# Performance work log

Measured on AMD Instinct MI355X. Metric: run time of the kernel, lower is better.

The kernel has to match this reference:

```python
import jax, jax.numpy as jnp
import numpy as np

MARGIN = 0.2
SCALE = 30.0

def setup_inputs() -> dict:
    key = jax.random.key(0)
    k1, k2 = jax.random.split(key)
    B, D, C = 8192, 512, 100
    embeddings = jax.random.normal(k1, (B, D), dtype=jnp.float32)
    labels = jax.random.randint(k2, (B,), 0, C, dtype=jnp.int64)
    return {"embeddings": embeddings, "labels": labels}

def reference(embeddings, labels):
    # Cosine similarity via one GEMM: normalize rows once, then n @ n.T.
    # (torch F.cosine_similarity uses eps=1e-8 on norms)
    norms = jnp.maximum(jnp.linalg.norm(embeddings, axis=1, keepdims=True), 1e-8)
    n = embeddings / norms                      # [B, D]
    sim = n @ n.T                               # [B, B]
    pos_mask = labels[:, None] == labels[None, :]  # includes diagonal, as in original
    e = jnp.exp(SCALE * (sim - MARGIN))         # [B, B]
    pos_sum = jnp.sum(jnp.where(pos_mask, e, 0.0))
    neg_sum = jnp.sum(jnp.where(pos_mask, 0.0, e))
    loss = jnp.log1p(neg_sum / pos_sum)
    return loss
```

## Files before the change

kernel.cpp:

```cpp
#include <hip/hip_runtime.h>
#include <hip/hip_bf16.h>
#include <math.h>


#define BDIM 8192
#define DDIM 512
#define MARGIN 0.2f
#define SCALE 30.0f

#define BT 256
#define BK 32
#define NKT (DDIM / BK)
#define NT (BDIM / BT)
#define NBLK (NT * (NT + 1) / 2)

typedef __hip_bfloat16 bf16;
using f32x4  = __attribute__((ext_vector_type(4))) float;
using bf16x8 = __attribute__((ext_vector_type(8))) short;
using us8    = __attribute__((ext_vector_type(8))) unsigned short;

#define GLOAD_LDS16(gp, lp)                                                    \
    __builtin_amdgcn_global_load_lds(                                          \
        (const __attribute__((address_space(1))) unsigned int*)(gp),           \
        (__attribute__((address_space(3))) unsigned int*)(lp), 16, 0, 0)

__device__ __forceinline__ unsigned short f2bf(float x) {
    union { bf16 h; unsigned short u; } c;
    c.h = __float2bfloat16(x);
    return c.u;
}

__global__ __launch_bounds__(256)
void norm_rows_kernel(const float* __restrict__ emb, bf16* __restrict__ nout,
                      double* __restrict__ accum, unsigned* __restrict__ ctr) {
    if (blockIdx.x == 0 && threadIdx.x == 0) {
        accum[0] = 0.0; accum[1] = 0.0; *ctr = 0u;
    }
    const int row  = blockIdx.x * 4 + (threadIdx.x >> 6);
    const int lane = threadIdx.x & 63;
    const float4* src = (const float4*)(emb + (size_t)row * DDIM) + lane * 2;
    const float4 a = src[0];
    const float4 b = src[1];
    float ss = a.x * a.x + a.y * a.y + a.z * a.z + a.w * a.w
             + b.x * b.x + b.y * b.y + b.z * b.z + b.w * b.w;
    #pragma unroll
    for (int off = 1; off < 64; off <<= 1) ss += __shfl_xor(ss, off, 64);
    const float inv = 1.0f / fmaxf(sqrtf(ss), 1e-8f);
    float v[8] = { a.x, a.y, a.z, a.w, b.x, b.y, b.z, b.w };
    us8 o;
    #pragma unroll
    for (int i = 0; i < 8; ++i) o[i] = f2bf(v[i] * inv);
    *((us8*)(nout + (size_t)row * DDIM) + lane) = o;
}

__global__ __launch_bounds__(512, 2)
void gemm_loss_kernel(const bf16* __restrict__ nmat,
                      const int* __restrict__ labels,
                      double* __restrict__ accum, unsigned* __restrict__ ctr,
                      float* __restrict__ out) {
    const int hw = blockIdx.x;
    const int l = (hw & 7) * (NBLK / 8) + (hw >> 3);
    auto tri = [](int b) { return ((65 - b) * b) >> 1; };
    int bi = (int)((65.0 - sqrt(4225.0 - 8.0 * (double)l)) * 0.5);
    bi = bi < 0 ? 0 : (bi > 31 ? 31 : bi);
    while (bi > 0 && tri(bi) > l) --bi;
    while (tri(bi + 1) <= l) ++bi;
    const int bj = bi + (l - tri(bi));

    __shared__ alignas(16) short As[4][BT * BK];
    __shared__ alignas(16) short Bs[4][BT * BK];
    __shared__ int lr[BT], lc[BT];
    __shared__ double red[16];

    const int tix = threadIdx.x, wid = tix >> 6, lane = tix & 63;
    if (tix < 256) lr[tix] = labels[bi * BT + tix];
    else           lc[tix - 256] = labels[bj * BT + (tix - 256)];

    const int wm = wid >> 2;
    const int wn = wid & 3;

    const int srow = wid * 16 + (lane >> 2);
    const int scol = ((lane & 3) ^ ((lane >> 3) & 3)) * 8;
    const bf16* gA = nmat + (size_t)(bi * BT + srow) * DDIM + scol;
    const bf16* gB = nmat + (size_t)(bj * BT + srow) * DDIM + scol;
    const int ldst = wid * 16 * BK;

    #define STG_A(buf, kt, h)                                                  \
        GLOAD_LDS16(gA + (size_t)((h) * 128) * DDIM + (kt) * BK,               \
                    &As[buf][(h) * 128 * BK + ldst])
    #define STG_B(buf, kt, h)                                                  \
        GLOAD_LDS16(gB + (size_t)((h) * 128) * DDIM + (kt) * BK,               \
                    &Bs[buf][(h) * 128 * BK + ldst])

    const int aoff  = (lane & 15) * BK + (((lane >> 4) ^ ((lane >> 1) & 3)) * 8);
    const int abase = wm * 128 * BK;
    const int bbase = wn * 64 * BK;

    f32x4 acc[8][4] = {};

    #pragma unroll
    for (int tt = 0; tt < 3; ++tt) {
        STG_A(tt, tt, 0); STG_A(tt, tt, 1);
        STG_B(tt, tt, 0); STG_B(tt, tt, 1);
    }
    asm volatile("s_waitcnt vmcnt(8)" ::: "memory");
    __builtin_amdgcn_s_barrier();
    asm volatile("" ::: "memory");

    #pragma unroll
    for (int t = 0; t < NKT; ++t) {
        const int cur = t & 3, pre = (t + 3) & 3;
        bf16x8 a[4], b[4];
        #pragma unroll
        for (int m = 0; m < 4; ++m)
            a[m] = *(const bf16x8*)&As[cur][abase + m * (16 * BK) + aoff];
        #pragma unroll
        for (int n = 0; n < 4; ++n)
            b[n] = *(const bf16x8*)&Bs[cur][bbase + n * (16 * BK) + aoff];
        if (t < NKT - 3) { STG_A(pre, t + 3, 0); STG_A(pre, t + 3, 1); }
        __builtin_amdgcn_s_barrier();
        asm volatile("s_waitcnt lgkmcnt(0)" ::: "memory");
        __builtin_amdgcn_sched_barrier(0);
        __builtin_amdgcn_s_setprio(1);
        #pragma unroll
        for (int m = 0; m < 4; ++m)
            #pragma unroll
            for (int n = 0; n < 4; ++n)
                acc[m][n] = __builtin_amdgcn_mfma_f32_16x16x32_bf16(
                    a[m], b[n], acc[m][n], 0, 0, 0);
        __builtin_amdgcn_s_setprio(0);
        #pragma unroll
        for (int m = 0; m < 4; ++m)
            a[m] = *(const bf16x8*)&As[cur][abase + (m + 4) * (16 * BK) + aoff];
        if (t < NKT - 3) { STG_B(pre, t + 3, 0); STG_B(pre, t + 3, 1); }
        if (t <= NKT - 4)      { asm volatile("s_waitcnt vmcnt(8)" ::: "memory"); }
        else if (t == NKT - 3) { asm volatile("s_waitcnt vmcnt(4)" ::: "memory"); }
        else if (t == NKT - 2) { asm volatile("s_waitcnt vmcnt(0)" ::: "memory"); }
        __builtin_amdgcn_s_barrier();
        asm volatile("s_waitcnt lgkmcnt(0)" ::: "memory");
        __builtin_amdgcn_sched_barrier(0);
        __builtin_amdgcn_s_setprio(1);
        #pragma unroll
        for (int m = 0; m < 4; ++m)
            #pragma unroll
            for (int n = 0; n < 4; ++n)
                acc[m + 4][n] = __builtin_amdgcn_mfma_f32_16x16x32_bf16(
                    a[m], b[n], acc[m + 4][n], 0, 0, 0);
        __builtin_amdgcn_s_setprio(0);
    }
    #undef STG_A
    #undef STG_B

    float posf = 0.0f, negf = 0.0f;
    const int rbase = wm * 128 + (lane >> 4) * 4;
    const int cbase = wn * 64 + (lane & 15);
    #pragma unroll
    for (int m = 0; m < 8; ++m) {
        #pragma unroll
        for (int n = 0; n < 4; ++n) {
            const int ljv = lc[cbase + n * 16];
            #pragma unroll
            for (int r = 0; r < 4; ++r) {
                const float e = __expf(fmaf(acc[m][n][r], SCALE, -SCALE * MARGIN));
                if (lr[rbase + m * 16 + r] == ljv) posf += e; else negf += e;
            }
        }
    }

    double dp = (double)posf, dn = (double)negf;
    #pragma unroll
    for (int o = 32; o > 0; o >>= 1) {
        dp += __shfl_down(dp, o, 64);
        dn += __shfl_down(dn, o, 64);
    }
    if (lane == 0) { red[wid * 2] = dp; red[wid * 2 + 1] = dn; }
    __syncthreads();
    if (tix == 0) {
        const double w = (bi == bj) ? 1.0 : 2.0;
        double p = 0.0, q = 0.0;
        #pragma unroll
        for (int i = 0; i < 8; ++i) { p += red[2 * i]; q += red[2 * i + 1]; }
        atomicAdd(&accum[0], p * w);
        atomicAdd(&accum[1], q * w);
        __threadfence();
        unsigned prev = atomicAdd(ctr, 1u);
        if (prev == NBLK - 1) {
            __threadfence();
            double pp = atomicAdd(&accum[0], 0.0);
            double qq = atomicAdd(&accum[1], 0.0);
            out[0] = (float)log1p(qq / pp);
        }
    }
}

extern "C" void kernel_launch(void* const* d_in, const int* in_sizes, int n_in,
                              void* d_out, int out_size, void* d_ws, size_t ws_size,
                              hipStream_t stream) {
    const float* emb  = (const float*)d_in[0];
    const int* labels = (const int*)d_in[1];
    float* out        = (float*)d_out;

    double* accum = (double*)d_ws;
    unsigned* ctr = (unsigned*)((char*)d_ws + 16);
    bf16* nmat    = (bf16*)((char*)d_ws + 256);

    norm_rows_kernel<<<BDIM / 4, 256, 0, stream>>>(emb, nmat, accum, ctr);
    gemm_loss_kernel<<<NBLK, 512, 0, stream>>>(nmat, labels, accum, ctr, out);
}
```

Measured before the change: 134.7 us.

## Shrink GEMM tiles to 128x128 with single-buffered LDS and supertile block ordering

Changes the fused GEMM+loss kernel from 256x256 tiles with 512 threads and a 4-stage async LDS pipeline to 128x128 tiles with 256 threads and a simple load-sync-compute loop. Block indices are remapped in 16x16 supertile groups of the upper triangle, aiming for better L2 locality and more blocks for load balance. This gives up the prefetch pipeline and halves per-block data reuse, so global/LDS traffic per FLOP roughly doubles and load latency is exposed at every barrier.

Result: slower. 172.7 us (+28.2%).

```diff
diff --git a/kernel.cpp b/kernel.cpp
--- a/kernel.cpp
+++ b/kernel.cpp
@@ -8,10 +8,10 @@
 #define MARGIN 0.2f
 #define SCALE 30.0f
 
-#define BT 256
+#define BM 128
 #define BK 32
 #define NKT (DDIM / BK)
-#define NT (BDIM / BT)
+#define NT (BDIM / BM)
 #define NBLK (NT * (NT + 1) / 2)
 
 typedef __hip_bfloat16 bf16;
@@ -53,109 +53,83 @@
     *((us8*)(nout + (size_t)row * DDIM) + lane) = o;
 }
 
-__global__ __launch_bounds__(512, 2)
+__global__ __launch_bounds__(256)
 void gemm_loss_kernel(const bf16* __restrict__ nmat,
                       const int* __restrict__ labels,
                       double* __restrict__ accum, unsigned* __restrict__ ctr,
                       float* __restrict__ out) {
-    const int hw = blockIdx.x;
-    const int l = (hw & 7) * (NBLK / 8) + (hw >> 3);
-    auto tri = [](int b) { return ((65 - b) * b) >> 1; };
-    int bi = (int)((65.0 - sqrt(4225.0 - 8.0 * (double)l)) * 0.5);
-    bi = bi < 0 ? 0 : (bi > 31 ? 31 : bi);
-    while (bi > 0 && tri(bi) > l) --bi;
-    while (tri(bi + 1) <= l) ++bi;
-    const int bj = bi + (l - tri(bi));
+    const int p = (blockIdx.x & 7) * (NBLK / 8) + (blockIdx.x >> 3);
+    const int scum[10] = {136, 392, 648, 904, 1040, 1296, 1552, 1688, 1944, 2080};
+    const int ssi[10]  = {0, 0, 0, 0, 1, 1, 1, 2, 2, 3};
+    const int ssj[10]  = {0, 1, 2, 3, 1, 2, 3, 2, 3, 3};
+    int s = 0;
+    while (p >= scum[s]) ++s;
+    const int q = p - (s ? scum[s - 1] : 0);
+    int bi, bj;
+    if (ssi[s] == ssj[s]) {
+        int r = 0;
+        while ((16 * (r + 1) - ((r + 1) * r) / 2) <= q) ++r;
+        const int rowbase = 16 * r - (r * (r - 1)) / 2;
+        bi = ssi[s] * 16 + r;
+        bj = ssj[s] * 16 + r + (q - rowbase);
+    } else {
+        bi = ssi[s] * 16 + (q >> 4);
+        bj = ssj[s] * 16 + (q & 15);
+    }
 
-    __shared__ alignas(16) short As[4][BT * BK];
-    __shared__ alignas(16) short Bs[4][BT * BK];
-    __shared__ int lr[BT], lc[BT];
-    __shared__ double red[16];
+    __shared__ alignas(16) short As[BM * BK];
+    __shared__ alignas(16) short Bs[BM * BK];
+    __shared__ int lr[BM], lc[BM];
+    __shared__ double red[8];
 
-    const int tix = threadIdx.x, wid = tix >> 6, lane = tix & 63;
-    if (tix < 256) lr[tix] = labels[bi * BT + tix];
-    else           lc[tix - 256] = labels[bj * BT + (tix - 256)];
+    const int t = threadIdx.x, wid = t >> 6, lane = t & 63;
+    if (t < 128) lr[t] = labels[bi * BM + t];
+    else         lc[t - 128] = labels[bj * BM + (t - 128)];
 
-    const int wm = wid >> 2;
-    const int wn = wid & 3;
+    const int wr = wid >> 1;
+    const int wc = wid & 1;
 
-    const int srow = wid * 16 + (lane >> 2);
+    const int srow = 16 * wid + (lane >> 2);
     const int scol = ((lane & 3) ^ ((lane >> 3) & 3)) * 8;
-    const bf16* gA = nmat + (size_t)(bi * BT + srow) * DDIM + scol;
-    const bf16* gB = nmat + (size_t)(bj * BT + srow) * DDIM + scol;
-    const int ldst = wid * 16 * BK;
-
-    #define STG_A(buf, kt, h)                                                  \
-        GLOAD_LDS16(gA + (size_t)((h) * 128) * DDIM + (kt) * BK,               \
-                    &As[buf][(h) * 128 * BK + ldst])
-    #define STG_B(buf, kt, h)                                                  \
-        GLOAD_LDS16(gB + (size_t)((h) * 128) * DDIM + (kt) * BK,               \
-                    &Bs[buf][(h) * 128 * BK + ldst])
+    const bf16* gA = nmat + (size_t)(bi * BM + srow) * DDIM + scol;
+    const bf16* gB = nmat + (size_t)(bj * BM + srow) * DDIM + scol;
+    const int ldst = (16 * wid) * BK;
 
     const int aoff  = (lane & 15) * BK + (((lane >> 4) ^ ((lane >> 1) & 3)) * 8);
-    const int abase = wm * 128 * BK;
-    const int bbase = wn * 64 * BK;
+    const int abase = (wr * 64) * BK;
+    const int bbase = (wc * 64) * BK;
 
-    f32x4 acc[8][4] = {};
+    f32x4 acc[4][4] = {};
 
-    #pragma unroll
-    for (int tt = 0; tt < 3; ++tt) {
-        STG_A(tt, tt, 0); STG_A(tt, tt, 1);
-        STG_B(tt, tt, 0); STG_B(tt, tt, 1);
-    }
-    asm volatile("s_waitcnt vmcnt(8)" ::: "memory");
-    __builtin_amdgcn_s_barrier();
-    asm volatile("" ::: "memory");
+    for (int kt = 0; kt < NKT; ++kt) {
+        const int k0 = kt * BK;
+        GLOAD_LDS16(gA + k0,                    &As[ldst]);
+        GLOAD_LDS16(gA + (size_t)64 * DDIM + k0, &As[64 * BK + ldst]);
+        GLOAD_LDS16(gB + k0,                    &Bs[ldst]);
+        GLOAD_LDS16(gB + (size_t)64 * DDIM + k0, &Bs[64 * BK + ldst]);
+        __syncthreads();
 
-    #pragma unroll
-    for (int t = 0; t < NKT; ++t) {
-        const int cur = t & 3, pre = (t + 3) & 3;
         bf16x8 a[4], b[4];
         #pragma unroll
         for (int m = 0; m < 4; ++m)
-            a[m] = *(const bf16x8*)&As[cur][abase + m * (16 * BK) + aoff];
+            a[m] = *(const bf16x8*)&As[abase + m * (16 * BK) + aoff];
         #pragma unroll
         for (int n = 0; n < 4; ++n)
-            b[n] = *(const bf16x8*)&Bs[cur][bbase + n * (16 * BK) + aoff];
-        if (t < NKT - 3) { STG_A(pre, t + 3, 0); STG_A(pre, t + 3, 1); }
-        __builtin_amdgcn_s_barrier();
-        asm volatile("s_waitcnt lgkmcnt(0)" ::: "memory");
-        __builtin_amdgcn_sched_barrier(0);
-        __builtin_amdgcn_s_setprio(1);
+            b[n] = *(const bf16x8*)&Bs[bbase + n * (16 * BK) + aoff];
         #pragma unroll
         for (int m = 0; m < 4; ++m)
             #pragma unroll
             for (int n = 0; n < 4; ++n)
                 acc[m][n] = __builtin_amdgcn_mfma_f32_16x16x32_bf16(
                     a[m], b[n], acc[m][n], 0, 0, 0);
-        __builtin_amdgcn_s_setprio(0);
-        #pragma unroll
-        for (int m = 0; m < 4; ++m)
-            a[m] = *(const bf16x8*)&As[cur][abase + (m + 4) * (16 * BK) + aoff];
-        if (t < NKT - 3) { STG_B(pre, t + 3, 0); STG_B(pre, t + 3, 1); }
-        if (t <= NKT - 4)      { asm volatile("s_waitcnt vmcnt(8)" ::: "memory"); }
-        else if (t == NKT - 3) { asm volatile("s_waitcnt vmcnt(4)" ::: "memory"); }
-        else if (t == NKT - 2) { asm volatile("s_waitcnt vmcnt(0)" ::: "memory"); }
-        __builtin_amdgcn_s_barrier();
-        asm volatile("s_waitcnt lgkmcnt(0)" ::: "memory");
-        __builtin_amdgcn_sched_barrier(0);
-        __builtin_amdgcn_s_setprio(1);
-        #pragma unroll
-        for (int m = 0; m < 4; ++m)
-            #pragma unroll
-            for (int n = 0; n < 4; ++n)
-                acc[m + 4][n] = __builtin_amdgcn_mfma_f32_16x16x32_bf16(
-                    a[m], b[n], acc[m + 4][n], 0, 0, 0);
-        __builtin_amdgcn_s_setprio(0);
+        __syncthreads();
     }
-    #undef STG_A
-    #undef STG_B
 
     float posf = 0.0f, negf = 0.0f;
-    const int rbase = wm * 128 + (lane >> 4) * 4;
-    const int cbase = wn * 64 + (lane & 15);
+    const int rbase = wr * 64 + (lane >> 4) * 4;
+    const int cbase = wc * 64 + (lane & 15);
     #pragma unroll
-    for (int m = 0; m < 8; ++m) {
+    for (int m = 0; m < 4; ++m) {
         #pragma unroll
         for (int n = 0; n < 4; ++n) {
             const int ljv = lc[cbase + n * 16];
@@ -175,20 +149,19 @@
     }
     if (lane == 0) { red[wid * 2] = dp; red[wid * 2 + 1] = dn; }
     __syncthreads();
-    if (tix == 0) {
+    if (t == 0) {
         const double w = (bi == bj) ? 1.0 : 2.0;
-        double p = 0.0, q = 0.0;
-        #pragma unroll
-        for (int i = 0; i < 8; ++i) { p += red[2 * i]; q += red[2 * i + 1]; }
-        atomicAdd(&accum[0], p * w);
-        atomicAdd(&accum[1], q * w);
+        double pp = (red[0] + red[2]) + (red[4] + red[6]);
+        double qq = (red[1] + red[3]) + (red[5] + red[7]);
+        atomicAdd(&accum[0], pp * w);
+        atomicAdd(&accum[1], qq * w);
         __threadfence();
         unsigned prev = atomicAdd(ctr, 1u);
         if (prev == NBLK - 1) {
             __threadfence();
-            double pp = atomicAdd(&accum[0], 0.0);
-            double qq = atomicAdd(&accum[1], 0.0);
-            out[0] = (float)log1p(qq / pp);
+            double ps = atomicAdd(&accum[0], 0.0);
+            double ns = atomicAdd(&accum[1], 0.0);
+            out[0] = (float)log1p(ns / ps);
         }
     }
 }
@@ -205,5 +178,5 @@
     bf16* nmat    = (bf16*)((char*)d_ws + 256);
 
     norm_rows_kernel<<<BDIM / 4, 256, 0, stream>>>(emb, nmat, accum, ctr);
-    gemm_loss_kernel<<<NBLK, 512, 0, stream>>>(nmat, labels, accum, ctr, out);
+    gemm_loss_kernel<<<NBLK, 256, 0, stream>>>(nmat, labels, accum, ctr, out);
 }
```
